# Kernel tuning notes

Hardware: AMD Instinct MI355X
Metric: run time of the kernel (lower is better)

The kernel has to match this reference:

```python
import jax, jax.numpy as jnp
import numpy as np

B, N, K = 32, 4096, 8          # batch, num input features (64x64 map), num slots
HID, D, DM = 256, 256, 512     # hid_dim, slot_dim, mlp_hid_dim
ITERS = 3
TEMP = 1.0
EPS = 1e-8
SCALE = D ** -0.5              # (slot_dim // num_heads) ** -0.5, heads=1


def layer_norm(x, g, b):
    m = jnp.mean(x, axis=-1, keepdims=True)
    v = jnp.mean((x - m) ** 2, axis=-1, keepdims=True)
    return (x - m) * jax.lax.rsqrt(v + 1e-5) * g + b


def setup_inputs() -> dict:
    key = jax.random.key(0)
    ks = jax.random.split(key, 20)
    s = 0.02
    inp = {
        "inputs": jax.random.normal(ks[0], (B, N, HID), jnp.float32),
        "noise": jax.random.normal(ks[1], (B, K, D), jnp.float32),
        "slots_mu": jax.random.normal(ks[2], (1, 1, D), jnp.float32),
        "slots_sigma": jnp.abs(jax.random.normal(ks[3], (1, 1, D), jnp.float32)),
        "ln_in_g": jnp.ones((HID,), jnp.float32),
        "ln_in_b": jnp.zeros((HID,), jnp.float32),
        "ln_slots_g": jnp.ones((D,), jnp.float32),
        "ln_slots_b": jnp.zeros((D,), jnp.float32),
        "ln_mlp_g": jnp.ones((D,), jnp.float32),
        "ln_mlp_b": jnp.zeros((D,), jnp.float32),
        # Linear weights stored [in, out]
        "Wq": jax.random.normal(ks[4], (D, D), jnp.float32) * s,
        "bq": jnp.zeros((D,), jnp.float32),
        "Wk": jax.random.normal(ks[5], (HID, D), jnp.float32) * s,
        "bk": jnp.zeros((D,), jnp.float32),
        "Wv": jax.random.normal(ks[6], (HID, D), jnp.float32) * s,
        "bv": jnp.zeros((D,), jnp.float32),
        # GRUCell params (torch layout transposed to [in, 3D])
        "W_ih": jax.random.normal(ks[7], (D, 3 * D), jnp.float32) * s,
        "W_hh": jax.random.normal(ks[8], (D, 3 * D), jnp.float32) * s,
        "b_ih": jnp.zeros((3 * D,), jnp.float32),
        "b_hh": jnp.zeros((3 * D,), jnp.float32),
        # residual MLP
        "W1": jax.random.normal(ks[9], (D, DM), jnp.float32) * s,
        "b1": jnp.zeros((DM,), jnp.float32),
        "W2": jax.random.normal(ks[10], (DM, D), jnp.float32) * s,
        "b2": jnp.zeros((D,), jnp.float32),
    }
    return inp


def reference(inputs, noise, slots_mu, slots_sigma,
              ln_in_g, ln_in_b, ln_slots_g, ln_slots_b, ln_mlp_g, ln_mlp_b,
              Wq, bq, Wk, bk, Wv, bv,
              W_ih, W_hh, b_ih, b_hh,
              W1, b1, W2, b2):
    x = layer_norm(inputs, ln_in_g, ln_in_b)            # [B,N,HID]
    k = x @ Wk + bk                                     # [B,N,D]
    v = x @ Wv + bv                                     # [B,N,D]

    slots = slots_mu + slots_sigma * noise              # [B,K,D]

    for _ in range(ITERS):
        slots_prev = slots
        s = layer_norm(slots, ln_slots_g, ln_slots_b)
        q = s @ Wq + bq                                  # [B,K,D]
        dots = jnp.einsum('bkd,bnd->bkn', q, k) * SCALE / TEMP
        attn = jax.nn.softmax(dots, axis=1)              # inverted: over slot axis
        attn = attn + EPS
        attn = attn / jnp.sum(attn, axis=2, keepdims=True)  # weighted mean over keys
        updates = jnp.einsum('bkn,bnd->bkd', attn, v)    # [B,K,D]

        # GRUCell on flattened (B*K, D)
        xg = updates.reshape(-1, D)
        h = slots_prev.reshape(-1, D)
        gi = xg @ W_ih + b_ih
        gh = h @ W_hh + b_hh
        i_r, i_z, i_n = jnp.split(gi, 3, axis=-1)
        h_r, h_z, h_n = jnp.split(gh, 3, axis=-1)
        r = jax.nn.sigmoid(i_r + h_r)
        z = jax.nn.sigmoid(i_z + h_z)
        n = jnp.tanh(i_n + r * h_n)
        h = (1.0 - z) * n + z * h
        slots = h.reshape(B, K, D)

        # residual MLP
        m = layer_norm(slots, ln_mlp_g, ln_mlp_b)
        slots = slots + (jax.nn.relu(m @ W1 + b1) @ W2 + b2)

    return slots
```

## Files before the change

### kernel.cpp

```cpp
#include <hip/hip_runtime.h>
#include <hip/hip_bf16.h>

#define NB 32
#define NPOS 4096
#define NSLOT 8
#define HIDD 256
#define DDIM 256
#define SCALE_F 0.0625f
#define EPS_F 1e-8f
#define NCHUNK 32
#define CPOS 128
#define TPOS 32

typedef __attribute__((ext_vector_type(4))) float f32x4;
typedef __attribute__((ext_vector_type(8))) short s16x8;
typedef __attribute__((ext_vector_type(2))) unsigned int u32x2;

__device__ __forceinline__ unsigned short f2bf(float f) {
    unsigned int x = __float_as_uint(f);
    x = (x + 0x7fffu + ((x >> 16) & 1u)) >> 16;
    return (unsigned short)x;
}
__device__ __forceinline__ float bf_lo(unsigned u) { return __uint_as_float(u << 16); }
__device__ __forceinline__ float bf_hi(unsigned u) { return __uint_as_float(u & 0xffff0000u); }

__global__ __launch_bounds__(256) void k_ln_in(
        const float* __restrict__ x, const float* __restrict__ g,
        const float* __restrict__ b, unsigned short* __restrict__ lnx) {
    int lane = threadIdx.x & 63;
    int wave = threadIdx.x >> 6;
    long row = (long)blockIdx.x * 4 + wave;
    const float4* xr = (const float4*)(x + row * 256);
    float4 v = xr[lane];
    float s = v.x + v.y + v.z + v.w;
    float sq = v.x * v.x + v.y * v.y + v.z * v.z + v.w * v.w;
    #pragma unroll
    for (int m = 32; m; m >>= 1) { s += __shfl_xor(s, m); sq += __shfl_xor(sq, m); }
    float mean = s * 0.00390625f;
    float rstd = rsqrtf(sq * 0.00390625f - mean * mean + 1e-5f);
    const float4 gg = ((const float4*)g)[lane];
    const float4 bb = ((const float4*)b)[lane];
    ushort4 o;
    o.x = f2bf((v.x - mean) * rstd * gg.x + bb.x);
    o.y = f2bf((v.y - mean) * rstd * gg.y + bb.y);
    o.z = f2bf((v.z - mean) * rstd * gg.z + bb.z);
    o.w = f2bf((v.w - mean) * rstd * gg.w + bb.w);
    ((ushort4*)(lnx + row * 256))[lane] = o;
}

__device__ __forceinline__ unsigned packrow(const float* __restrict__ W, int hp, int N, int c) {
    return (unsigned)f2bf(W[(2*hp)*N + c]) | ((unsigned)f2bf(W[(2*hp+1)*N + c]) << 16);
}

__global__ __launch_bounds__(256) void k_prep(
        const float* __restrict__ Wq, const float* __restrict__ Wk,
        const float* __restrict__ Wv, const float* __restrict__ Wih,
        const float* __restrict__ Whh, const float* __restrict__ W1,
        const float* __restrict__ W2,
        unsigned* __restrict__ WqP, unsigned* __restrict__ WkTP,
        unsigned* __restrict__ WvP, unsigned* __restrict__ WihP,
        unsigned* __restrict__ WhhP, unsigned* __restrict__ W1P,
        unsigned* __restrict__ W2P) {
    int i = blockIdx.x * 256 + threadIdx.x;
    if (i < 32768) {
        int hp = i >> 8, c = i & 255;
        WqP[i] = packrow(Wq, hp, 256, c);
        WvP[i] = packrow(Wv, hp, 256, c);
        WkTP[i] = (unsigned)f2bf(Wk[c*256 + 2*hp]) | ((unsigned)f2bf(Wk[c*256 + 2*hp + 1]) << 16);
    }
    if (i < 65536) {
        int hp1 = i >> 9, c1 = i & 511;
        W1P[i] = packrow(W1, hp1, 512, c1);
        int hp2 = i >> 8, c2 = i & 255;
        W2P[i] = packrow(W2, hp2, 256, c2);
    }
    if (i < 98304) {
        int hp = i / 768, c = i % 768;
        WihP[i] = packrow(Wih, hp, 768, c);
        WhhP[i] = packrow(Whh, hp, 768, c);
    }
}

__device__ __forceinline__ void qk_tail(
        float v0, float v1, int b, int s0,
        const float* __restrict__ lng, const float* __restrict__ lnb,
        const float* __restrict__ Wq, const float* __restrict__ bq,
        const float* __restrict__ Wk, const float* __restrict__ bk,
        unsigned short* __restrict__ qkg, float* __restrict__ qbkg,
        float (*sh)[256], float (*red)[4]) {
    int c = threadIdx.x;
    float s_0 = v0, q_0 = v0 * v0, s_1 = v1, q_1 = v1 * v1;
    #pragma unroll
    for (int m = 32; m; m >>= 1) {
        s_0 += __shfl_xor(s_0, m); q_0 += __shfl_xor(q_0, m);
        s_1 += __shfl_xor(s_1, m); q_1 += __shfl_xor(q_1, m);
    }
    if ((c & 63) == 0) { int w = c >> 6; red[w][0]=s_0; red[w][1]=q_0; red[w][2]=s_1; red[w][3]=q_1; }
    __syncthreads();
    float S0 = red[0][0]+red[1][0]+red[2][0]+red[3][0];
    float Q0 = red[0][1]+red[1][1]+red[2][1]+red[3][1];
    float S1 = red[0][2]+red[1][2]+red[2][2]+red[3][2];
    float Q1 = red[0][3]+red[1][3]+red[2][3]+red[3][3];
    float m0 = S0 * 0.00390625f, r0 = rsqrtf(Q0 * 0.00390625f - m0*m0 + 1e-5f);
    float m1 = S1 * 0.00390625f, r1 = rsqrtf(Q1 * 0.00390625f - m1*m1 + 1e-5f);
    float gc = lng[c], bc = lnb[c];
    sh[0][c] = (v0 - m0) * r0 * gc + bc;
    sh[1][c] = (v1 - m1) * r1 * gc + bc;
    __syncthreads();
    float qa0 = bq[c], qa1 = qa0;
    for (int h = 0; h < 256; h += 4) {
        float w0 = Wq[(h+0)*256+c], w1 = Wq[(h+1)*256+c];
        float w2 = Wq[(h+2)*256+c], w3 = Wq[(h+3)*256+c];
        float4 x0 = *(const float4*)&sh[0][h], x1 = *(const float4*)&sh[1][h];
        qa0 += x0.x*w0 + x0.y*w1 + x0.z*w2 + x0.w*w3;
        qa1 += x1.x*w0 + x1.y*w1 + x1.z*w2 + x1.w*w3;
    }
    __syncthreads();
    sh[0][c] = qa0; sh[1][c] = qa1;
    float bkc = bk[c];
    float p0 = qa0 * bkc, p1 = qa1 * bkc;
    #pragma unroll
    for (int m = 32; m; m >>= 1) { p0 += __shfl_xor(p0, m); p1 += __shfl_xor(p1, m); }
    __syncthreads();
    if ((c & 63) == 0) { int w = c >> 6; red[w][0] = p0; red[w][1] = p1; }
    __syncthreads();
    if (c < 2) qbkg[b*8 + s0 + c] = SCALE_F * (red[0][c]+red[1][c]+red[2][c]+red[3][c]);
    float k0 = 0.f, k1 = 0.f;
    const float* wkr = Wk + (long)c * 256;
    for (int d = 0; d < 256; d += 4) {
        float4 wk4 = *(const float4*)&wkr[d];
        float4 x0 = *(const float4*)&sh[0][d], x1 = *(const float4*)&sh[1][d];
        k0 += x0.x*wk4.x + x0.y*wk4.y + x0.z*wk4.z + x0.w*wk4.w;
        k1 += x1.x*wk4.x + x1.y*wk4.y + x1.z*wk4.z + x1.w*wk4.w;
    }
    qkg[(b*8 + s0    )*256 + c] = f2bf(SCALE_F * k0);
    qkg[(b*8 + s0 + 1)*256 + c] = f2bf(SCALE_F * k1);
}

__global__ __launch_bounds__(256) void k_init(
        const float* __restrict__ noise, const float* __restrict__ mu,
        const float* __restrict__ sig, const float* __restrict__ lng,
        const float* __restrict__ lnb, const float* __restrict__ Wq,
        const float* __restrict__ bq, const float* __restrict__ Wk,
        const float* __restrict__ bk, float* __restrict__ slots,
        unsigned short* __restrict__ qkg, float* __restrict__ qbkg) {
    __shared__ float sh[2][256];
    __shared__ float red[4][4];
    int b = blockIdx.x >> 2, rp = blockIdx.x & 3;
    int s0 = rp * 2, r0 = b * 8 + s0;
    int c = threadIdx.x;
    float v0 = mu[c] + sig[c] * noise[r0*256 + c];
    float v1 = mu[c] + sig[c] * noise[(r0+1)*256 + c];
    slots[r0*256 + c] = v0;
    slots[(r0+1)*256 + c] = v1;
    qk_tail(v0, v1, b, s0, lng, lnb, Wq, bq, Wk, bk, qkg, qbkg, sh, red);
}

__global__ __launch_bounds__(128) void k_stream(
        const unsigned short* __restrict__ lnx, const unsigned short* __restrict__ qk,
        const float* __restrict__ qbk, float* __restrict__ Upart,
        float* __restrict__ dpart) {
    __shared__ unsigned short xt[TPOS * 256];
    __shared__ float Ured[8 * 256];
    __shared__ float dred[8];
    int b = blockIdx.x >> 5, ch = blockIdx.x & 31;
    int t = threadIdx.x;
    int l = t & 63, w = t >> 6;
    for (int i = t; i < 2048; i += 128) Ured[i] = 0.f;
    if (t < 8) dred[t] = 0.f;
    int slot = l & 15, g = l >> 4;
    s16x8 qkf[8];
    float qbkv = 0.f;
    if (slot < 8) {
        const unsigned short* qrow = qk + (b*8 + slot) * 256;
        #pragma unroll
        for (int hk = 0; hk < 8; hk++)
            qkf[hk] = *(const s16x8*)(qrow + hk*32 + 8*g);
        qbkv = qbk[b*8 + slot];
    } else {
        #pragma unroll
        for (int hk = 0; hk < 8; hk++) qkf[hk] = (s16x8)0;
    }
    f32x4 uacc[16];
    #pragma unroll
    for (int i = 0; i < 16; i++) uacc[i] = (f32x4)0.f;
    float dreg = 0.f;
    int gbase = (b * NPOS + ch * CPOS) * 256;
    int pw = w * 16;
    __syncthreads();
    for (int tile = 0; tile < 4; tile++) {
        #pragma unroll
        for (int i = 0; i < 8; i++) {
            int c = t + 128 * i;
            int p = c >> 5, hc = c & 31;
            int4 v = *(const int4*)(lnx + gbase + (tile*TPOS + p)*256 + hc*8);
            *(int4*)&xt[p*256 + ((hc ^ (p & 15)) << 3)] = v;
        }
        __syncthreads();
        f32x4 acc = (f32x4)0.f;
        {
            int prow = pw + (l & 15);
            const unsigned short* xrow = &xt[prow * 256];
            int sw = prow & 15;
            #pragma unroll
            for (int hk = 0; hk < 8; hk++) {
                s16x8 a = *(const s16x8*)(xrow + (((hk*4 + g) ^ sw) << 3));
                acc = __builtin_amdgcn_mfma_f32_16x16x32_bf16(a, qkf[hk], acc, 0, 0, 0);
            }
        }
        float at[4];
        #pragma unroll
        for (int r = 0; r < 4; r++) {
            float v = acc[r] + qbkv;
            float m = v;
            m = fmaxf(m, __shfl_xor(m, 1));
            m = fmaxf(m, __shfl_xor(m, 2));
            m = fmaxf(m, __shfl_xor(m, 4));
            float e = __expf(v - m);
            float sum = e;
            sum += __shfl_xor(sum, 1);
            sum += __shfl_xor(sum, 2);
            sum += __shfl_xor(sum, 4);
            float a = e / sum;
            at[r] = a;
            dreg += a;
        }
        u32x2 a2;
        a2.x = (unsigned)f2bf(at[0]) | ((unsigned)f2bf(at[1]) << 16);
        a2.y = (unsigned)f2bf(at[2]) | ((unsigned)f2bf(at[3]) << 16);
        int p0 = pw + 4 * g;
        int hl = l & 7;
        #pragma unroll
        for (int hc = 0; hc < 16; hc++) {
            int hcol = hc * 2 + ((l & 15) >> 3);
            unsigned e0 = xt[(p0+0)*256 + ((hcol ^ ((p0+0) & 15)) << 3) + hl];
            unsigned e1 = xt[(p0+1)*256 + ((hcol ^ ((p0+1) & 15)) << 3) + hl];
            unsigned e2 = xt[(p0+2)*256 + ((hcol ^ ((p0+2) & 15)) << 3) + hl];
            unsigned e3 = xt[(p0+3)*256 + ((hcol ^ ((p0+3) & 15)) << 3) + hl];
            u32x2 b2;
            b2.x = e0 | (e1 << 16);
            b2.y = e2 | (e3 << 16);
            asm volatile("v_mfma_f32_16x16x16_bf16 %0, %1, %2, %0"
                         : "+v"(uacc[hc]) : "v"(a2), "v"(b2));
        }
        __syncthreads();
    }
    if (g < 2) {
        #pragma unroll
        for (int hc = 0; hc < 16; hc++) {
            int h = hc * 16 + (l & 15);
            #pragma unroll
            for (int r = 0; r < 4; r++)
                atomicAdd(&Ured[(4*g + r)*256 + h], uacc[hc][r]);
        }
    }
    dreg += __shfl_xor(dreg, 16);
    dreg += __shfl_xor(dreg, 32);
    if (slot < 8 && g == 0) atomicAdd(&dred[slot], dreg);
    __syncthreads();
    float* up = Upart + (long)(b * NCHUNK + ch) * 2048;
    for (int i = t; i < 2048; i += 128) up[i] = Ured[i];
    if (t < 8) dpart[(b * NCHUNK + ch) * 8 + t] = dred[t];
}

__device__ __forceinline__ float ln1024(float v, int c, const float* __restrict__ g,
                                        const float* __restrict__ b, float (*red)[2]) {
    float s1 = v, s2 = v * v;
    #pragma unroll
    for (int m = 32; m; m >>= 1) { s1 += __shfl_xor(s1, m); s2 += __shfl_xor(s2, m); }
    int w = threadIdx.x >> 6;
    if ((threadIdx.x & 63) == 0) { red[w][0] = s1; red[w][1] = s2; }
    __syncthreads();
    float S = 0.f, Q = 0.f;
    #pragma unroll
    for (int i = 0; i < 16; i++) { S += red[i][0]; Q += red[i][1]; }
    float mean = S * (1.f/1024.f);
    float rstd = rsqrtf(Q * (1.f/1024.f) - mean*mean + 1e-5f);
    __syncthreads();
    return (v - mean) * rstd * g[c] + b[c];
}

__global__ __launch_bounds__(1024) void k_post(
        const float* __restrict__ Upart, const float* __restrict__ dpart,
        const unsigned* __restrict__ WvP, const float* __restrict__ bv,
        const unsigned* __restrict__ WihP, const unsigned* __restrict__ WhhP,
        const float* __restrict__ bih, const float* __restrict__ bhh,
        const float* __restrict__ lnmg, const float* __restrict__ lnmb,
        const unsigned* __restrict__ W1P, const float* __restrict__ b1,
        const unsigned* __restrict__ W2P, const float* __restrict__ b2,
        const float* __restrict__ lnsg, const float* __restrict__ lnsb,
        const unsigned* __restrict__ WqP, const float* __restrict__ bq,
        const unsigned* __restrict__ WkTP, const float* __restrict__ bk,
        float* __restrict__ slots, unsigned short* __restrict__ qkg,
        float* __restrict__ qbkg, float* __restrict__ outp, int last) {
    __shared__ float A[256];
    __shared__ float B[256];
    __shared__ float P4[4][256];
    __shared__ float G[12][256];
    __shared__ float H2[2][512];
    __shared__ float H[512];
    __shared__ float red[16][2];
    __shared__ float scal[1];
    int r = blockIdx.x, b = r >> 3, s = r & 7;
    int t = threadIdx.x, c = t & 255, q = t >> 8;
    {
        float u = 0.f;
        const float* ub = Upart + (long)b * NCHUNK * 2048 + s * 256 + c;
        #pragma unroll
        for (int i = 0; i < 8; i++) u += ub[(q * 8 + i) * 2048];
        P4[q][c] = u;
        if (q == 1) B[c] = slots[r * 256 + c];
        if (t < 32) {
            float dv = dpart[(b * NCHUNK + t) * 8 + s];
            #pragma unroll
            for (int m = 16; m; m >>= 1) dv += __shfl_xor(dv, m);
            if (t == 0) scal[0] = dv;
        }
    }
    __syncthreads();
    float dn = 1.f / (scal[0] + (float)NPOS * EPS_F);
    if (q == 0) A[c] = P4[0][c] + P4[1][c] + P4[2][c] + P4[3][c];
    __syncthreads();
    {
        float acc = 0.f;
        const unsigned* wp = WvP + q * 32 * 256 + c;
        const float* ap = A + q * 64;
        #pragma unroll 8
        for (int i = 0; i < 32; i++) {
            unsigned wv = wp[i * 256];
            acc += ap[2*i] * bf_lo(wv) + ap[2*i+1] * bf_hi(wv);
        }
        P4[q][c] = acc;
    }
    __syncthreads();
    float updc = (P4[0][c] + P4[1][c] + P4[2][c] + P4[3][c]) * dn + bv[c];
    if (q == 0) A[c] = updc;
    __syncthreads();
    {
        const float* src = (q < 2) ? A : B;
        const unsigned* W = (q < 2) ? WihP : WhhP;
        int base = (q & 1) * 64;
        float ar = 0.f, az = 0.f, an = 0.f;
        #pragma unroll 4
        for (int i = 0; i < 64; i++) {
            int hp = base + i;
            float a0 = src[2*hp], a1 = src[2*hp+1];
            unsigned w0 = W[hp*768 + c];
            unsigned w1 = W[hp*768 + c + 256];
            unsigned w2 = W[hp*768 + c + 512];
            ar += a0*bf_lo(w0) + a1*bf_hi(w0);
            az += a0*bf_lo(w1) + a1*bf_hi(w1);
            an += a0*bf_lo(w2) + a1*bf_hi(w2);
        }
        G[q*3+0][c] = ar; G[q*3+1][c] = az; G[q*3+2][c] = an;
    }
    __syncthreads();
    float spc = B[c];
    float gir = bih[c]     + G[0][c] + G[3][c];
    float giz = bih[c+256] + G[1][c] + G[4][c];
    float gin = bih[c+512] + G[2][c] + G[5][c];
    float ghr = bhh[c]     + G[6][c] + G[9][c];
    float ghz = bhh[c+256] + G[7][c] + G[10][c];
    float ghn = bhh[c+512] + G[8][c] + G[11][c];
    float rg = 1.f/(1.f + __expf(-(gir+ghr)));
    float zg = 1.f/(1.f + __expf(-(giz+ghz)));
    float ng = tanhf(gin + rg*ghn);
    float hnew = (1.f - zg)*ng + zg*spc;
    float mmc = ln1024(hnew, c, lnmg, lnmb, red);
    if (q == 0) A[c] = mmc;
    __syncthreads();
    {
        int j = t & 511, kh = t >> 9;
        float acc = 0.f;
        #pragma unroll 8
        for (int i = 0; i < 64; i++) {
            int hp = kh*64 + i;
            unsigned wv = W1P[hp*512 + j];
            acc += A[2*hp]*bf_lo(wv) + A[2*hp+1]*bf_hi(wv);
        }
        H2[kh][j] = acc;
    }
    __syncthreads();
    if (t < 512) H[t] = fmaxf(H2[0][t] + H2[1][t] + b1[t], 0.f);
    __syncthreads();
    {
        float acc = 0.f;
        const unsigned* wp = W2P + q * 64 * 256 + c;
        const float* hb = H + q * 128;
        #pragma unroll 8
        for (int i = 0; i < 64; i++) {
            unsigned wv = wp[i * 256];
            acc += hb[2*i]*bf_lo(wv) + hb[2*i+1]*bf_hi(wv);
        }
        P4[q][c] = acc;
    }
    __syncthreads();
    float outc = hnew + P4[0][c] + P4[1][c] + P4[2][c] + P4[3][c] + b2[c];
    if (t < 256) {
        slots[r*256 + c] = outc;
        if (last) outp[r*256 + c] = outc;
    }
    if (last) return;
    float sc = ln1024(outc, c, lnsg, lnsb, red);
    if (q == 0) A[c] = sc;
    __syncthreads();
    {
        float acc = 0.f;
        const unsigned* wp = WqP + q * 32 * 256 + c;
        const float* ap = A + q * 64;
        #pragma unroll 8
        for (int i = 0; i < 32; i++) {
            unsigned wv = wp[i * 256];
            acc += ap[2*i]*bf_lo(wv) + ap[2*i+1]*bf_hi(wv);
        }
        P4[q][c] = acc;
    }
    __syncthreads();
    float qc = P4[0][c] + P4[1][c] + P4[2][c] + P4[3][c] + bq[c];
    {
        float v = qc * bk[c];
        #pragma unroll
        for (int m = 32; m; m >>= 1) v += __shfl_xor(v, m);
        int w = t >> 6;
        if ((t & 63) == 0) red[w][0] = v;
        __syncthreads();
        if (t == 0) {
            float S = 0.f;
            #pragma unroll
            for (int i = 0; i < 16; i++) S += red[i][0];
            qbkg[r] = SCALE_F * 0.25f * S;
        }
    }
    if (q == 0) A[c] = qc;
    __syncthreads();
    {
        float acc = 0.f;
        const unsigned* wp = WkTP + q * 32 * 256 + c;
        const float* ap = A + q * 64;
        #pragma unroll 8
        for (int i = 0; i < 32; i++) {
            unsigned wv = wp[i * 256];
            acc += ap[2*i]*bf_lo(wv) + ap[2*i+1]*bf_hi(wv);
        }
        P4[q][c] = acc;
    }
    __syncthreads();
    if (t < 256) qkg[r*256 + c] = f2bf(SCALE_F * (P4[0][c] + P4[1][c] + P4[2][c] + P4[3][c]));
}

extern "C" void kernel_launch(void* const* d_in, const int* in_sizes, int n_in,
                              void* d_out, int out_size, void* d_ws, size_t ws_size,
                              hipStream_t stream) {
    const float* inputs = (const float*)d_in[0];
    const float* noise  = (const float*)d_in[1];
    const float* mu     = (const float*)d_in[2];
    const float* sig    = (const float*)d_in[3];
    const float* lnig   = (const float*)d_in[4];
    const float* lnib   = (const float*)d_in[5];
    const float* lnsg   = (const float*)d_in[6];
    const float* lnsb   = (const float*)d_in[7];
    const float* lnmg   = (const float*)d_in[8];
    const float* lnmb   = (const float*)d_in[9];
    const float* Wq     = (const float*)d_in[10];
    const float* bq     = (const float*)d_in[11];
    const float* Wk     = (const float*)d_in[12];
    const float* bk     = (const float*)d_in[13];
    const float* Wv     = (const float*)d_in[14];
    const float* bv     = (const float*)d_in[15];
    const float* Wih    = (const float*)d_in[16];
    const float* Whh    = (const float*)d_in[17];
    const float* bih    = (const float*)d_in[18];
    const float* bhh    = (const float*)d_in[19];
    const float* W1     = (const float*)d_in[20];
    const float* b1     = (const float*)d_in[21];
    const float* W2     = (const float*)d_in[22];
    const float* b2     = (const float*)d_in[23];

    char* ws = (char*)d_ws;
    unsigned short* lnx = (unsigned short*)ws;
    size_t off = (size_t)NB * NPOS * HIDD * 2;
    unsigned short* qkb = (unsigned short*)(ws + off); off += (size_t)NB*NSLOT*HIDD*2;
    float* qbk   = (float*)(ws + off); off += (size_t)NB*NSLOT*4;
    float* Upart = (float*)(ws + off); off += (size_t)NB*NCHUNK*NSLOT*HIDD*4;
    float* dpart = (float*)(ws + off); off += (size_t)NB*NCHUNK*NSLOT*4;
    float* slots = (float*)(ws + off); off += (size_t)NB*NSLOT*DDIM*4;
    unsigned* WqP  = (unsigned*)(ws + off); off += 32768u*4;
    unsigned* WkTP = (unsigned*)(ws + off); off += 32768u*4;
    unsigned* WvP  = (unsigned*)(ws + off); off += 32768u*4;
    unsigned* WihP = (unsigned*)(ws + off); off += 98304u*4;
    unsigned* WhhP = (unsigned*)(ws + off); off += 98304u*4;
    unsigned* W1P  = (unsigned*)(ws + off); off += 65536u*4;
    unsigned* W2P  = (unsigned*)(ws + off); off += 65536u*4;

    k_prep<<<384, 256, 0, stream>>>(Wq, Wk, Wv, Wih, Whh, W1, W2,
                                    WqP, WkTP, WvP, WihP, WhhP, W1P, W2P);
    k_ln_in<<<NB*NPOS/4, 256, 0, stream>>>(inputs, lnig, lnib, lnx);
    k_init<<<NB*4, 256, 0, stream>>>(noise, mu, sig, lnsg, lnsb, Wq, bq, Wk, bk,
                                     slots, qkb, qbk);
    for (int it = 0; it < 3; it++) {
        k_stream<<<NB*NCHUNK, 128, 0, stream>>>(lnx, qkb, qbk, Upart, dpart);
        k_post<<<NB*NSLOT, 1024, 0, stream>>>(Upart, dpart,
                                              WvP, bv, WihP, WhhP, bih, bhh,
                                              lnmg, lnmb, W1P, b1, W2P, b2,
                                              lnsg, lnsb, WqP, bq, WkTP, bk,
                                              slots, qkb, qbk, (float*)d_out,
                                              it == 2 ? 1 : 0);
    }
}
```

Before: 242.9 us.

## Vectorize k_post matvecs with 16-byte weight loads and finer K-split reductions

Each matrix-vector product in the per-slot post kernel now has every thread load four packed bf16 weight columns with one uint4 access. The input dimension is split into 8 or 16 groups instead of 2 or 4, and the partial sums are reduced through a larger shared-memory union. The aim is fewer, wider global loads and more memory-level parallelism in the weight-bandwidth-bound GRU, MLP and q/k projections. In exchange it adds extra shared-memory reduction passes and barriers, and uses more LDS per block.

```diff
diff --git a/kernel.cpp b/kernel.cpp
--- a/kernel.cpp
+++ b/kernel.cpp
@@ -23,6 +23,13 @@
 }
 __device__ __forceinline__ float bf_lo(unsigned u) { return __uint_as_float(u << 16); }
 __device__ __forceinline__ float bf_hi(unsigned u) { return __uint_as_float(u & 0xffff0000u); }
+
+__device__ __forceinline__ void fma4(f32x4& acc, uint4 wv, float a0, float a1) {
+    acc[0] += a0 * bf_lo(wv.x) + a1 * bf_hi(wv.x);
+    acc[1] += a0 * bf_lo(wv.y) + a1 * bf_hi(wv.y);
+    acc[2] += a0 * bf_lo(wv.z) + a1 * bf_hi(wv.z);
+    acc[3] += a0 * bf_lo(wv.w) + a1 * bf_hi(wv.w);
+}
 
 __global__ __launch_bounds__(256) void k_ln_in(
         const float* __restrict__ x, const float* __restrict__ g,
@@ -293,22 +300,22 @@
         const unsigned* __restrict__ WkTP, const float* __restrict__ bk,
         float* __restrict__ slots, unsigned short* __restrict__ qkg,
         float* __restrict__ qbkg, float* __restrict__ outp, int last) {
-    __shared__ float A[256];
-    __shared__ float B[256];
-    __shared__ float P4[4][256];
-    __shared__ float G[12][256];
-    __shared__ float H2[2][512];
-    __shared__ float H[512];
+    __shared__ union {
+        float PG[2][8][768];
+        struct { float P16[16][256]; float H2[8][512]; } s;
+    } sm;
+    __shared__ float A[256], B[256], G2[2][768], H[512];
     __shared__ float red[16][2];
     __shared__ float scal[1];
     int r = blockIdx.x, b = r >> 3, s = r & 7;
     int t = threadIdx.x, c = t & 255, q = t >> 8;
+    int cg = t & 63, kg16 = t >> 6;
     {
         float u = 0.f;
         const float* ub = Upart + (long)b * NCHUNK * 2048 + s * 256 + c;
         #pragma unroll
         for (int i = 0; i < 8; i++) u += ub[(q * 8 + i) * 2048];
-        P4[q][c] = u;
+        sm.s.P16[q][c] = u;
         if (q == 1) B[c] = slots[r * 256 + c];
         if (t < 32) {
             float dv = dpart[(b * NCHUNK + t) * 8 + s];
@@ -319,49 +326,66 @@
     }
     __syncthreads();
     float dn = 1.f / (scal[0] + (float)NPOS * EPS_F);
-    if (q == 0) A[c] = P4[0][c] + P4[1][c] + P4[2][c] + P4[3][c];
-    __syncthreads();
-    {
-        float acc = 0.f;
-        const unsigned* wp = WvP + q * 32 * 256 + c;
-        const float* ap = A + q * 64;
-        #pragma unroll 8
-        for (int i = 0; i < 32; i++) {
-            unsigned wv = wp[i * 256];
-            acc += ap[2*i] * bf_lo(wv) + ap[2*i+1] * bf_hi(wv);
-        }
-        P4[q][c] = acc;
-    }
-    __syncthreads();
-    float updc = (P4[0][c] + P4[1][c] + P4[2][c] + P4[3][c]) * dn + bv[c];
-    if (q == 0) A[c] = updc;
-    __syncthreads();
-    {
-        const float* src = (q < 2) ? A : B;
-        const unsigned* W = (q < 2) ? WihP : WhhP;
-        int base = (q & 1) * 64;
-        float ar = 0.f, az = 0.f, an = 0.f;
+    if (q == 0) A[c] = sm.s.P16[0][c] + sm.s.P16[1][c] + sm.s.P16[2][c] + sm.s.P16[3][c];
+    __syncthreads();
+    {
+        f32x4 acc = (f32x4)0.f;
+        const uint4* wp = (const uint4*)(WvP + kg16 * 8 * 256 + 4 * cg);
+        #pragma unroll
+        for (int i = 0; i < 8; i++) {
+            uint4 wv = wp[i * 64];
+            fma4(acc, wv, A[2*(kg16*8+i)], A[2*(kg16*8+i)+1]);
+        }
+        *(f32x4*)&sm.s.P16[kg16][4*cg] = acc;
+    }
+    __syncthreads();
+    float updtmp;
+    {
+        float ss = 0.f;
+        #pragma unroll
+        for (int k = 0; k < 16; k++) ss += sm.s.P16[k][c];
+        updtmp = ss * dn + bv[c];
+    }
+    __syncthreads();
+    if (q == 0) A[c] = updtmp;
+    __syncthreads();
+    {
+        int h = t >> 9;
+        int kg = (t >> 6) & 7;
+        const float* src = h ? B : A;
+        const unsigned* W = h ? WhhP : WihP;
+        f32x4 ar = (f32x4)0.f, az = (f32x4)0.f, an = (f32x4)0.f;
         #pragma unroll 4
-        for (int i = 0; i < 64; i++) {
-            int hp = base + i;
+        for (int i = 0; i < 16; i++) {
+            int hp = kg * 16 + i;
             float a0 = src[2*hp], a1 = src[2*hp+1];
-            unsigned w0 = W[hp*768 + c];
-            unsigned w1 = W[hp*768 + c + 256];
-            unsigned w2 = W[hp*768 + c + 512];
-            ar += a0*bf_lo(w0) + a1*bf_hi(w0);
-            az += a0*bf_lo(w1) + a1*bf_hi(w1);
-            an += a0*bf_lo(w2) + a1*bf_hi(w2);
-        }
-        G[q*3+0][c] = ar; G[q*3+1][c] = az; G[q*3+2][c] = an;
+            uint4 w0 = *(const uint4*)(W + hp*768 + 4*cg);
+            uint4 w1 = *(const uint4*)(W + hp*768 + 256 + 4*cg);
+            uint4 w2 = *(const uint4*)(W + hp*768 + 512 + 4*cg);
+            fma4(ar, w0, a0, a1);
+            fma4(az, w1, a0, a1);
+            fma4(an, w2, a0, a1);
+        }
+        *(f32x4*)&sm.PG[h][kg][4*cg]       = ar;
+        *(f32x4*)&sm.PG[h][kg][256 + 4*cg] = az;
+        *(f32x4*)&sm.PG[h][kg][512 + 4*cg] = an;
+    }
+    __syncthreads();
+    for (int idx = t; idx < 1536; idx += 1024) {
+        int h = idx / 768, cc = idx - h * 768;
+        float ss = 0.f;
+        #pragma unroll
+        for (int k = 0; k < 8; k++) ss += sm.PG[h][k][cc];
+        G2[h][cc] = ss;
     }
     __syncthreads();
     float spc = B[c];
-    float gir = bih[c]     + G[0][c] + G[3][c];
-    float giz = bih[c+256] + G[1][c] + G[4][c];
-    float gin = bih[c+512] + G[2][c] + G[5][c];
-    float ghr = bhh[c]     + G[6][c] + G[9][c];
-    float ghz = bhh[c+256] + G[7][c] + G[10][c];
-    float ghn = bhh[c+512] + G[8][c] + G[11][c];
+    float gir = bih[c]     + G2[0][c];
+    float giz = bih[c+256] + G2[0][c+256];
+    float gin = bih[c+512] + G2[0][c+512];
+    float ghr = bhh[c]     + G2[1][c];
+    float ghz = bhh[c+256] + G2[1][c+256];
+    float ghn = bhh[c+512] + G2[1][c+512];
     float rg = 1.f/(1.f + __expf(-(gir+ghr)));
     float zg = 1.f/(1.f + __expf(-(giz+ghz)));
     float ng = tanhf(gin + rg*ghn);
@@ -370,53 +394,69 @@
     if (q == 0) A[c] = mmc;
     __syncthreads();
     {
-        int j = t & 511, kh = t >> 9;
-        float acc = 0.f;
-        #pragma unroll 8
-        for (int i = 0; i < 64; i++) {
-            int hp = kh*64 + i;
-            unsigned wv = W1P[hp*512 + j];
-            acc += A[2*hp]*bf_lo(wv) + A[2*hp+1]*bf_hi(wv);
-        }
-        H2[kh][j] = acc;
-    }
-    __syncthreads();
-    if (t < 512) H[t] = fmaxf(H2[0][t] + H2[1][t] + b1[t], 0.f);
-    __syncthreads();
-    {
-        float acc = 0.f;
-        const unsigned* wp = W2P + q * 64 * 256 + c;
-        const float* hb = H + q * 128;
-        #pragma unroll 8
-        for (int i = 0; i < 64; i++) {
-            unsigned wv = wp[i * 256];
-            acc += hb[2*i]*bf_lo(wv) + hb[2*i+1]*bf_hi(wv);
-        }
-        P4[q][c] = acc;
-    }
-    __syncthreads();
-    float outc = hnew + P4[0][c] + P4[1][c] + P4[2][c] + P4[3][c] + b2[c];
+        int kg = t >> 7, cg1 = t & 127;
+        f32x4 acc = (f32x4)0.f;
+        const uint4* wp = (const uint4*)(W1P + kg * 16 * 512 + 4 * cg1);
+        #pragma unroll 4
+        for (int i = 0; i < 16; i++) {
+            uint4 wv = wp[i * 128];
+            fma4(acc, wv, A[2*(kg*16+i)], A[2*(kg*16+i)+1]);
+        }
+        *(f32x4*)&sm.s.H2[kg][4*cg1] = acc;
+    }
+    __syncthreads();
+    if (t < 512) {
+        float ss = b1[t];
+        #pragma unroll
+        for (int k = 0; k < 8; k++) ss += sm.s.H2[k][t];
+        H[t] = fmaxf(ss, 0.f);
+    }
+    __syncthreads();
+    {
+        f32x4 acc = (f32x4)0.f;
+        const uint4* wp = (const uint4*)(W2P + kg16 * 16 * 256 + 4 * cg);
+        #pragma unroll 4
+        for (int i = 0; i < 16; i++) {
+            uint4 wv = wp[i * 64];
+            fma4(acc, wv, H[2*(kg16*16+i)], H[2*(kg16*16+i)+1]);
+        }
+        *(f32x4*)&sm.s.P16[kg16][4*cg] = acc;
+    }
+    __syncthreads();
+    float outc;
+    {
+        float ss = 0.f;
+        #pragma unroll
+        for (int k = 0; k < 16; k++) ss += sm.s.P16[k][c];
+        outc = hnew + ss + b2[c];
+    }
     if (t < 256) {
         slots[r*256 + c] = outc;
         if (last) outp[r*256 + c] = outc;
     }
     if (last) return;
+    __syncthreads();
     float sc = ln1024(outc, c, lnsg, lnsb, red);
     if (q == 0) A[c] = sc;
     __syncthreads();
     {
-        float acc = 0.f;
-        const unsigned* wp = WqP + q * 32 * 256 + c;
-        const float* ap = A + q * 64;
-        #pragma unroll 8
-        for (int i = 0; i < 32; i++) {
-            unsigned wv = wp[i * 256];
-            acc += ap[2*i]*bf_lo(wv) + ap[2*i+1]*bf_hi(wv);
-        }
-        P4[q][c] = acc;
-    }
-    __syncthreads();
-    float qc = P4[0][c] + P4[1][c] + P4[2][c] + P4[3][c] + bq[c];
+        f32x4 acc = (f32x4)0.f;
+        const uint4* wp = (const uint4*)(WqP + kg16 * 8 * 256 + 4 * cg);
+        #pragma unroll
+        for (int i = 0; i < 8; i++) {
+            uint4 wv = wp[i * 64];
+            fma4(acc, wv, A[2*(kg16*8+i)], A[2*(kg16*8+i)+1]);
+        }
+        *(f32x4*)&sm.s.P16[kg16][4*cg] = acc;
+    }
+    __syncthreads();
+    float qc;
+    {
+        float ss = 0.f;
+        #pragma unroll
+        for (int k = 0; k < 16; k++) ss += sm.s.P16[k][c];
+        qc = ss + bq[c];
+    }
     {
         float v = qc * bk[c];
         #pragma unroll
@@ -430,22 +470,27 @@
             for (int i = 0; i < 16; i++) S += red[i][0];
             qbkg[r] = SCALE_F * 0.25f * S;
         }
+        __syncthreads();
     }
     if (q == 0) A[c] = qc;
     __syncthreads();
     {
-        float acc = 0.f;
-        const unsigned* wp = WkTP + q * 32 * 256 + c;
-        const float* ap = A + q * 64;
-        #pragma unroll 8
-        for (int i = 0; i < 32; i++) {
-            unsigned wv = wp[i * 256];
-            acc += ap[2*i]*bf_lo(wv) + ap[2*i+1]*bf_hi(wv);
-        }
-        P4[q][c] = acc;
-    }
-    __syncthreads();
-    if (t < 256) qkg[r*256 + c] = f2bf(SCALE_F * (P4[0][c] + P4[1][c] + P4[2][c] + P4[3][c]));
+        f32x4 acc = (f32x4)0.f;
+        const uint4* wp = (const uint4*)(WkTP + kg16 * 8 * 256 + 4 * cg);
+        #pragma unroll
+        for (int i = 0; i < 8; i++) {
+            uint4 wv = wp[i * 64];
+            fma4(acc, wv, A[2*(kg16*8+i)], A[2*(kg16*8+i)+1]);
+        }
+        *(f32x4*)&sm.s.P16[kg16][4*cg] = acc;
+    }
+    __syncthreads();
+    if (t < 256) {
+        float ss = 0.f;
+        #pragma unroll
+        for (int k = 0; k < 16; k++) ss += sm.s.P16[k][c];
+        qkg[r*256 + c] = f2bf(SCALE_F * ss);
+    }
 }
 
 extern "C" void kernel_launch(void* const* d_in, const int* in_sizes, int n_in,
```

Result: faster. 236.6 us (-2.6%).

## Fold Wq·Wkᵀ into one matrix, batch 4 slots per post block, use fp16 dot2

Applied to the files above, without the earlier changes.

Precomputes the fused query-key projection M = Wq·Wkᵀ plus the bias terms once in the prep kernel, so the post kernel does one matvec for q·K where it used to do two. The post kernel now handles 4 slots per 1024-thread block (64 blocks instead of 256), so each weight load is reused across 4 slots. The matvecs use packed fp16 weights and fdot2 instead of bf16 unpacking. This reduces weight traffic and instruction count in the serial per-iteration post step. In exchange it uses far fewer blocks and fp16 for weights and activations, which risks overflow or precision loss.

```diff
diff --git a/kernel.cpp b/kernel.cpp
--- a/kernel.cpp
+++ b/kernel.cpp
@@ -15,14 +15,21 @@
 typedef __attribute__((ext_vector_type(4))) float f32x4;
 typedef __attribute__((ext_vector_type(8))) short s16x8;
 typedef __attribute__((ext_vector_type(2))) unsigned int u32x2;
+typedef _Float16 h16x2 __attribute__((ext_vector_type(2)));
 
 __device__ __forceinline__ unsigned short f2bf(float f) {
     unsigned int x = __float_as_uint(f);
     x = (x + 0x7fffu + ((x >> 16) & 1u)) >> 16;
     return (unsigned short)x;
 }
-__device__ __forceinline__ float bf_lo(unsigned u) { return __uint_as_float(u << 16); }
-__device__ __forceinline__ float bf_hi(unsigned u) { return __uint_as_float(u & 0xffff0000u); }
+__device__ __forceinline__ unsigned short f2h(float f) {
+    _Float16 h = (_Float16)f;
+    return __builtin_bit_cast(unsigned short, h);
+}
+__device__ __forceinline__ unsigned pack2h(float a, float b) {
+    return (unsigned)f2h(a) | ((unsigned)f2h(b) << 16);
+}
+__device__ __forceinline__ h16x2 u2h(unsigned u) { return __builtin_bit_cast(h16x2, u); }
 
 __global__ __launch_bounds__(256) void k_ln_in(
         const float* __restrict__ x, const float* __restrict__ g,
@@ -48,48 +55,89 @@
     ((ushort4*)(lnx + row * 256))[lane] = o;
 }
 
-__device__ __forceinline__ unsigned packrow(const float* __restrict__ W, int hp, int N, int c) {
-    return (unsigned)f2bf(W[(2*hp)*N + c]) | ((unsigned)f2bf(W[(2*hp+1)*N + c]) << 16);
+__device__ __forceinline__ unsigned packrowh(const float* __restrict__ W, int hp, int N, int c) {
+    return pack2h(W[(2*hp)*N + c], W[(2*hp+1)*N + c]);
+}
+__device__ __forceinline__ float blkred(float v, float* red4) {
+    #pragma unroll
+    for (int m = 32; m; m >>= 1) v += __shfl_xor(v, m);
+    int w = threadIdx.x >> 6;
+    if ((threadIdx.x & 63) == 0) red4[w] = v;
+    __syncthreads();
+    float s = red4[0] + red4[1] + red4[2] + red4[3];
+    __syncthreads();
+    return s;
 }
 
 __global__ __launch_bounds__(256) void k_prep(
-        const float* __restrict__ Wq, const float* __restrict__ Wk,
         const float* __restrict__ Wv, const float* __restrict__ Wih,
         const float* __restrict__ Whh, const float* __restrict__ W1,
-        const float* __restrict__ W2,
-        unsigned* __restrict__ WqP, unsigned* __restrict__ WkTP,
+        const float* __restrict__ W2, const float* __restrict__ Wq,
+        const float* __restrict__ Wk, const float* __restrict__ bq,
+        const float* __restrict__ bk,
         unsigned* __restrict__ WvP, unsigned* __restrict__ WihP,
         unsigned* __restrict__ WhhP, unsigned* __restrict__ W1P,
-        unsigned* __restrict__ W2P) {
-    int i = blockIdx.x * 256 + threadIdx.x;
-    if (i < 32768) {
-        int hp = i >> 8, c = i & 255;
-        WqP[i] = packrow(Wq, hp, 256, c);
-        WvP[i] = packrow(Wv, hp, 256, c);
-        WkTP[i] = (unsigned)f2bf(Wk[c*256 + 2*hp]) | ((unsigned)f2bf(Wk[c*256 + 2*hp + 1]) << 16);
-    }
-    if (i < 65536) {
-        int hp1 = i >> 9, c1 = i & 511;
-        W1P[i] = packrow(W1, hp1, 512, c1);
-        int hp2 = i >> 8, c2 = i & 255;
-        W2P[i] = packrow(W2, hp2, 256, c2);
-    }
-    if (i < 98304) {
-        int hp = i / 768, c = i % 768;
-        WihP[i] = packrow(Wih, hp, 768, c);
-        WhhP[i] = packrow(Whh, hp, 768, c);
+        unsigned* __restrict__ W2P, unsigned* __restrict__ M1P,
+        float* __restrict__ v1, float* __restrict__ w2, float* __restrict__ sc2) {
+    int t = threadIdx.x;
+    if (blockIdx.x < 384) {
+        int i = blockIdx.x * 256 + t;
+        if (i < 32768) {
+            int hp = i >> 8, c = i & 255;
+            WvP[i] = packrowh(Wv, hp, 256, c);
+        }
+        if (i < 65536) {
+            int hp1 = i >> 9, c1 = i & 511;
+            W1P[i] = packrowh(W1, hp1, 512, c1);
+            int hp2 = i >> 8, c2 = i & 255;
+            W2P[i] = packrowh(W2, hp2, 256, c2);
+        }
+        if (i < 98304) {
+            int hp = i / 768, c = i % 768;
+            WihP[i] = packrowh(Wih, hp, 768, c);
+            WhhP[i] = packrowh(Whh, hp, 768, c);
+        }
+        return;
+    }
+    __shared__ float wq0[256], wq1[256], bqL[256];
+    __shared__ float red4[4];
+    int e2 = blockIdx.x - 384;
+    wq0[t] = Wq[(2*e2)*256 + t];
+    wq1[t] = Wq[(2*e2+1)*256 + t];
+    bqL[t] = bq[t];
+    __syncthreads();
+    const float4* wkr = (const float4*)(Wk + (long)t * 256);
+    float a0 = 0.f, a1 = 0.f;
+    for (int d = 0; d < 64; d++) {
+        float4 k4 = wkr[d];
+        a0 += wq0[4*d]*k4.x + wq0[4*d+1]*k4.y + wq0[4*d+2]*k4.z + wq0[4*d+3]*k4.w;
+        a1 += wq1[4*d]*k4.x + wq1[4*d+1]*k4.y + wq1[4*d+2]*k4.z + wq1[4*d+3]*k4.w;
+    }
+    M1P[e2*256 + t] = pack2h(a0, a1);
+    float p0 = blkred(wq0[t] * bk[t], red4);
+    float p1 = blkred(wq1[t] * bk[t], red4);
+    if (t == 0) { w2[2*e2] = p0; w2[2*e2+1] = p1; }
+    if (e2 == 0) {
+        float av = 0.f;
+        for (int d = 0; d < 64; d++) {
+            float4 k4 = wkr[d];
+            av += bqL[4*d]*k4.x + bqL[4*d+1]*k4.y + bqL[4*d+2]*k4.z + bqL[4*d+3]*k4.w;
+        }
+        v1[t] = av;
+        float p2 = blkred(bqL[t] * bk[t], red4);
+        if (t == 0) sc2[0] = p2;
     }
 }
 
 __device__ __forceinline__ void qk_tail(
-        float v0, float v1, int b, int s0,
+        float v0, float v1_, int b, int s0,
         const float* __restrict__ lng, const float* __restrict__ lnb,
         const float* __restrict__ Wq, const float* __restrict__ bq,
         const float* __restrict__ Wk, const float* __restrict__ bk,
         unsigned short* __restrict__ qkg, float* __restrict__ qbkg,
         float (*sh)[256], float (*red)[4]) {
     int c = threadIdx.x;
-    float s_0 = v0, q_0 = v0 * v0, s_1 = v1, q_1 = v1 * v1;
+    float s_0 = v0, q_0 = v0 * v0, s_1 = v1_, q_1 = v1_ * v1_;
     #pragma unroll
     for (int m = 32; m; m >>= 1) {
         s_0 += __shfl_xor(s_0, m); q_0 += __shfl_xor(q_0, m);
@@ -105,15 +153,15 @@
     float m1 = S1 * 0.00390625f, r1 = rsqrtf(Q1 * 0.00390625f - m1*m1 + 1e-5f);
     float gc = lng[c], bc = lnb[c];
     sh[0][c] = (v0 - m0) * r0 * gc + bc;
-    sh[1][c] = (v1 - m1) * r1 * gc + bc;
+    sh[1][c] = (v1_ - m1) * r1 * gc + bc;
     __syncthreads();
     float qa0 = bq[c], qa1 = qa0;
     for (int h = 0; h < 256; h += 4) {
         float w0 = Wq[(h+0)*256+c], w1 = Wq[(h+1)*256+c];
-        float w2 = Wq[(h+2)*256+c], w3 = Wq[(h+3)*256+c];
+        float w2_ = Wq[(h+2)*256+c], w3 = Wq[(h+3)*256+c];
         float4 x0 = *(const float4*)&sh[0][h], x1 = *(const float4*)&sh[1][h];
-        qa0 += x0.x*w0 + x0.y*w1 + x0.z*w2 + x0.w*w3;
-        qa1 += x1.x*w0 + x1.y*w1 + x1.z*w2 + x1.w*w3;
+        qa0 += x0.x*w0 + x0.y*w1 + x0.z*w2_ + x0.w*w3;
+        qa1 += x1.x*w0 + x1.y*w1 + x1.z*w2_ + x1.w*w3;
     }
     __syncthreads();
     sh[0][c] = qa0; sh[1][c] = qa1;
@@ -263,19 +311,19 @@
     if (t < 8) dpart[(b * NCHUNK + ch) * 8 + t] = dred[t];
 }
 
-__device__ __forceinline__ float ln1024(float v, int c, const float* __restrict__ g,
-                                        const float* __restrict__ b, float (*red)[2]) {
+__device__ __forceinline__ float ln4r(float v, int s, int c, int w,
+                                      const float* __restrict__ g,
+                                      const float* __restrict__ b,
+                                      float (*red)[2]) {
     float s1 = v, s2 = v * v;
     #pragma unroll
     for (int m = 32; m; m >>= 1) { s1 += __shfl_xor(s1, m); s2 += __shfl_xor(s2, m); }
-    int w = threadIdx.x >> 6;
     if ((threadIdx.x & 63) == 0) { red[w][0] = s1; red[w][1] = s2; }
     __syncthreads();
-    float S = 0.f, Q = 0.f;
-    #pragma unroll
-    for (int i = 0; i < 16; i++) { S += red[i][0]; Q += red[i][1]; }
-    float mean = S * (1.f/1024.f);
-    float rstd = rsqrtf(Q * (1.f/1024.f) - mean*mean + 1e-5f);
+    float S = red[4*s][0] + red[4*s+1][0] + red[4*s+2][0] + red[4*s+3][0];
+    float Q = red[4*s][1] + red[4*s+1][1] + red[4*s+2][1] + red[4*s+3][1];
+    float mean = S * 0.00390625f;
+    float rstd = rsqrtf(Q * 0.00390625f - mean*mean + 1e-5f);
     __syncthreads();
     return (v - mean) * rstd * g[c] + b[c];
 }
@@ -289,163 +337,123 @@
         const unsigned* __restrict__ W1P, const float* __restrict__ b1,
         const unsigned* __restrict__ W2P, const float* __restrict__ b2,
         const float* __restrict__ lnsg, const float* __restrict__ lnsb,
-        const unsigned* __restrict__ WqP, const float* __restrict__ bq,
-        const unsigned* __restrict__ WkTP, const float* __restrict__ bk,
+        const unsigned* __restrict__ M1P, const float* __restrict__ v1,
+        const float* __restrict__ w2g, const float* __restrict__ sc2g,
         float* __restrict__ slots, unsigned short* __restrict__ qkg,
         float* __restrict__ qbkg, float* __restrict__ outp, int last) {
-    __shared__ float A[256];
-    __shared__ float B[256];
-    __shared__ float P4[4][256];
-    __shared__ float G[12][256];
-    __shared__ float H2[2][512];
-    __shared__ float H[512];
+    __shared__ float Us[4][256], sl[4][256], hn[4][256], mm[4][256];
+    __shared__ float Hh[4][512];
+    __shared__ unsigned ap[4][128], apS[4][128], apH[4][256];
     __shared__ float red[16][2];
-    __shared__ float scal[1];
-    int r = blockIdx.x, b = r >> 3, s = r & 7;
-    int t = threadIdx.x, c = t & 255, q = t >> 8;
+    __shared__ float dnl[4];
+    int b = blockIdx.x >> 1, sh = blockIdx.x & 1, s0 = sh * 4;
+    int t = threadIdx.x, c = t & 255, s = t >> 8, w = t >> 6;
     {
         float u = 0.f;
-        const float* ub = Upart + (long)b * NCHUNK * 2048 + s * 256 + c;
-        #pragma unroll
-        for (int i = 0; i < 8; i++) u += ub[(q * 8 + i) * 2048];
-        P4[q][c] = u;
-        if (q == 1) B[c] = slots[r * 256 + c];
-        if (t < 32) {
-            float dv = dpart[(b * NCHUNK + t) * 8 + s];
-            #pragma unroll
-            for (int m = 16; m; m >>= 1) dv += __shfl_xor(dv, m);
-            if (t == 0) scal[0] = dv;
-        }
-    }
-    __syncthreads();
-    float dn = 1.f / (scal[0] + (float)NPOS * EPS_F);
-    if (q == 0) A[c] = P4[0][c] + P4[1][c] + P4[2][c] + P4[3][c];
-    __syncthreads();
-    {
-        float acc = 0.f;
-        const unsigned* wp = WvP + q * 32 * 256 + c;
-        const float* ap = A + q * 64;
+        const float* ub = Upart + ((long)b * 256 + s0 + s) * 256 + c;
         #pragma unroll 8
-        for (int i = 0; i < 32; i++) {
-            unsigned wv = wp[i * 256];
-            acc += ap[2*i] * bf_lo(wv) + ap[2*i+1] * bf_hi(wv);
-        }
-        P4[q][c] = acc;
-    }
-    __syncthreads();
-    float updc = (P4[0][c] + P4[1][c] + P4[2][c] + P4[3][c]) * dn + bv[c];
-    if (q == 0) A[c] = updc;
-    __syncthreads();
-    {
-        const float* src = (q < 2) ? A : B;
-        const unsigned* W = (q < 2) ? WihP : WhhP;
-        int base = (q & 1) * 64;
-        float ar = 0.f, az = 0.f, an = 0.f;
-        #pragma unroll 4
-        for (int i = 0; i < 64; i++) {
-            int hp = base + i;
-            float a0 = src[2*hp], a1 = src[2*hp+1];
-            unsigned w0 = W[hp*768 + c];
-            unsigned w1 = W[hp*768 + c + 256];
-            unsigned w2 = W[hp*768 + c + 512];
-            ar += a0*bf_lo(w0) + a1*bf_hi(w0);
-            az += a0*bf_lo(w1) + a1*bf_hi(w1);
-            an += a0*bf_lo(w2) + a1*bf_hi(w2);
-        }
-        G[q*3+0][c] = ar; G[q*3+1][c] = az; G[q*3+2][c] = an;
-    }
-    __syncthreads();
-    float spc = B[c];
-    float gir = bih[c]     + G[0][c] + G[3][c];
-    float giz = bih[c+256] + G[1][c] + G[4][c];
-    float gin = bih[c+512] + G[2][c] + G[5][c];
-    float ghr = bhh[c]     + G[6][c] + G[9][c];
-    float ghz = bhh[c+256] + G[7][c] + G[10][c];
-    float ghn = bhh[c+512] + G[8][c] + G[11][c];
-    float rg = 1.f/(1.f + __expf(-(gir+ghr)));
-    float zg = 1.f/(1.f + __expf(-(giz+ghz)));
-    float ng = tanhf(gin + rg*ghn);
-    float hnew = (1.f - zg)*ng + zg*spc;
-    float mmc = ln1024(hnew, c, lnmg, lnmb, red);
-    if (q == 0) A[c] = mmc;
-    __syncthreads();
-    {
-        int j = t & 511, kh = t >> 9;
+        for (int ch = 0; ch < 32; ch++) u += ub[ch * 2048];
+        Us[s][c] = u;
+        sl[s][c] = slots[(b*8 + s0 + s)*256 + c];
+        if (t < 4) {
+            float d = 0.f;
+            for (int ch = 0; ch < 32; ch++) d += dpart[(b*32 + ch)*8 + s0 + t];
+            dnl[t] = 1.f / (d + (float)NPOS * EPS_F);
+        }
+    }
+    __syncthreads();
+    if (t < 512) { int ss = t >> 7, dp = t & 127; ap[ss][dp]  = pack2h(Us[ss][2*dp], Us[ss][2*dp+1]); }
+    else         { int ss = (t-512) >> 7, dp = t & 127; apS[ss][dp] = pack2h(sl[ss][2*dp], sl[ss][2*dp+1]); }
+    __syncthreads();
+    {
         float acc = 0.f;
         #pragma unroll 8
-        for (int i = 0; i < 64; i++) {
-            int hp = kh*64 + i;
-            unsigned wv = W1P[hp*512 + j];
-            acc += A[2*hp]*bf_lo(wv) + A[2*hp+1]*bf_hi(wv);
-        }
-        H2[kh][j] = acc;
-    }
-    __syncthreads();
-    if (t < 512) H[t] = fmaxf(H2[0][t] + H2[1][t] + b1[t], 0.f);
-    __syncthreads();
+        for (int dp = 0; dp < 128; dp++)
+            acc = __builtin_amdgcn_fdot2(u2h(ap[s][dp]), u2h(WvP[dp*256 + c]), acc, false);
+        mm[s][c] = acc * dnl[s] + bv[c];
+    }
+    __syncthreads();
+    if (t < 512) { int ss = t >> 7, dp = t & 127; ap[ss][dp] = pack2h(mm[ss][2*dp], mm[ss][2*dp+1]); }
+    __syncthreads();
+    float hnew;
+    {
+        float gir = bih[c], giz = bih[c+256], gin = bih[c+512];
+        float ghr = bhh[c], ghz = bhh[c+256], ghn = bhh[c+512];
+        const unsigned* wi = WihP + c;
+        const unsigned* wh = WhhP + c;
+        #pragma unroll 2
+        for (int dp = 0; dp < 128; dp++) {
+            h16x2 au = u2h(ap[s][dp]);
+            h16x2 as_ = u2h(apS[s][dp]);
+            gir = __builtin_amdgcn_fdot2(au, u2h(wi[dp*768]),       gir, false);
+            giz = __builtin_amdgcn_fdot2(au, u2h(wi[dp*768 + 256]), giz, false);
+            gin = __builtin_amdgcn_fdot2(au, u2h(wi[dp*768 + 512]), gin, false);
+            ghr = __builtin_amdgcn_fdot2(as_, u2h(wh[dp*768]),       ghr, false);
+            ghz = __builtin_amdgcn_fdot2(as_, u2h(wh[dp*768 + 256]), ghz, false);
+            ghn = __builtin_amdgcn_fdot2(as_, u2h(wh[dp*768 + 512]), ghn, false);
+        }
+        float rg = 1.f/(1.f + __expf(-(gir+ghr)));
+        float zg = 1.f/(1.f + __expf(-(giz+ghz)));
+        float ng = tanhf(gin + rg*ghn);
+        hnew = (1.f - zg)*ng + zg*sl[s][c];
+        hn[s][c] = hnew;
+    }
+    __syncthreads();
+    {
+        float mmv = ln4r(hnew, s, c, w, lnmg, lnmb, red);
+        mm[s][c] = mmv;
+    }
+    __syncthreads();
+    if (t < 512) { int ss = t >> 7, dp = t & 127; ap[ss][dp] = pack2h(mm[ss][2*dp], mm[ss][2*dp+1]); }
+    __syncthreads();
+    {
+        int j = t & 511, sp = t >> 9;
+        float a0 = b1[j], a1 = b1[j];
+        #pragma unroll 4
+        for (int dp = 0; dp < 128; dp++) {
+            h16x2 wv = u2h(W1P[dp*512 + j]);
+            a0 = __builtin_amdgcn_fdot2(u2h(ap[sp*2][dp]),   wv, a0, false);
+            a1 = __builtin_amdgcn_fdot2(u2h(ap[sp*2+1][dp]), wv, a1, false);
+        }
+        Hh[sp*2][j]   = fmaxf(a0, 0.f);
+        Hh[sp*2+1][j] = fmaxf(a1, 0.f);
+    }
+    __syncthreads();
+    { int hp = t & 255; apH[s][hp] = pack2h(Hh[s][2*hp], Hh[s][2*hp+1]); }
+    __syncthreads();
+    float outc;
     {
         float acc = 0.f;
-        const unsigned* wp = W2P + q * 64 * 256 + c;
-        const float* hb = H + q * 128;
         #pragma unroll 8
-        for (int i = 0; i < 64; i++) {
-            unsigned wv = wp[i * 256];
-            acc += hb[2*i]*bf_lo(wv) + hb[2*i+1]*bf_hi(wv);
-        }
-        P4[q][c] = acc;
-    }
-    __syncthreads();
-    float outc = hnew + P4[0][c] + P4[1][c] + P4[2][c] + P4[3][c] + b2[c];
-    if (t < 256) {
-        slots[r*256 + c] = outc;
-        if (last) outp[r*256 + c] = outc;
-    }
-    if (last) return;
-    float sc = ln1024(outc, c, lnsg, lnsb, red);
-    if (q == 0) A[c] = sc;
-    __syncthreads();
-    {
-        float acc = 0.f;
-        const unsigned* wp = WqP + q * 32 * 256 + c;
-        const float* ap = A + q * 64;
+        for (int hp = 0; hp < 256; hp++)
+            acc = __builtin_amdgcn_fdot2(u2h(apH[s][hp]), u2h(W2P[hp*256 + c]), acc, false);
+        outc = hn[s][c] + acc + b2[c];
+    }
+    slots[(b*8 + s0 + s)*256 + c] = outc;
+    if (last) { outp[(b*8 + s0 + s)*256 + c] = outc; return; }
+    __syncthreads();
+    {
+        float sc = ln4r(outc, s, c, w, lnsg, lnsb, red);
+        mm[s][c] = sc;
+        float qv = sc * w2g[c];
+        #pragma unroll
+        for (int m = 32; m; m >>= 1) qv += __shfl_xor(qv, m);
+        if ((t & 63) == 0) red[w][0] = qv;
+    }
+    __syncthreads();
+    if (t < 512) { int ss = t >> 7, dp = t & 127; ap[ss][dp] = pack2h(mm[ss][2*dp], mm[ss][2*dp+1]); }
+    if ((t & 255) == 0) {
+        float S = red[4*s][0] + red[4*s+1][0] + red[4*s+2][0] + red[4*s+3][0];
+        qbkg[b*8 + s0 + s] = SCALE_F * (S + sc2g[0]);
+    }
+    __syncthreads();
+    {
+        float acc = v1[c];
         #pragma unroll 8
-        for (int i = 0; i < 32; i++) {
-            unsigned wv = wp[i * 256];
-            acc += ap[2*i]*bf_lo(wv) + ap[2*i+1]*bf_hi(wv);
-        }
-        P4[q][c] = acc;
-    }
-    __syncthreads();
-    float qc = P4[0][c] + P4[1][c] + P4[2][c] + P4[3][c] + bq[c];
-    {
-        float v = qc * bk[c];
-        #pragma unroll
-        for (int m = 32; m; m >>= 1) v += __shfl_xor(v, m);
-        int w = t >> 6;
-        if ((t & 63) == 0) red[w][0] = v;
-        __syncthreads();
-        if (t == 0) {
-            float S = 0.f;
-            #pragma unroll
-            for (int i = 0; i < 16; i++) S += red[i][0];
-            qbkg[r] = SCALE_F * 0.25f * S;
-        }
-    }
-    if (q == 0) A[c] = qc;
-    __syncthreads();
-    {
-        float acc = 0.f;
-        const unsigned* wp = WkTP + q * 32 * 256 + c;
-        const float* ap = A + q * 64;
-        #pragma unroll 8
-        for (int i = 0; i < 32; i++) {
-            unsigned wv = wp[i * 256];
-            acc += ap[2*i]*bf_lo(wv) + ap[2*i+1]*bf_hi(wv);
-        }
-        P4[q][c] = acc;
-    }
-    __syncthreads();
-    if (t < 256) qkg[r*256 + c] = f2bf(SCALE_F * (P4[0][c] + P4[1][c] + P4[2][c] + P4[3][c]));
+        for (int dp = 0; dp < 128; dp++)
+            acc = __builtin_amdgcn_fdot2(u2h(ap[s][dp]), u2h(M1P[dp*256 + c]), acc, false);
+        qkg[(b*8 + s0 + s)*256 + c] = f2bf(SCALE_F * acc);
+    }
 }
 
 extern "C" void kernel_launch(void* const* d_in, const int* in_sizes, int n_in,
@@ -484,26 +492,28 @@
     float* Upart = (float*)(ws + off); off += (size_t)NB*NCHUNK*NSLOT*HIDD*4;
     float* dpart = (float*)(ws + off); off += (size_t)NB*NCHUNK*NSLOT*4;
     float* slots = (float*)(ws + off); off += (size_t)NB*NSLOT*DDIM*4;
-    unsigned* WqP  = (unsigned*)(ws + off); off += 32768u*4;
-    unsigned* WkTP = (unsigned*)(ws + off); off += 32768u*4;
     unsigned* WvP  = (unsigned*)(ws + off); off += 32768u*4;
     unsigned* WihP = (unsigned*)(ws + off); off += 98304u*4;
     unsigned* WhhP = (unsigned*)(ws + off); off += 98304u*4;
     unsigned* W1P  = (unsigned*)(ws + off); off += 65536u*4;
     unsigned* W2P  = (unsigned*)(ws + off); off += 65536u*4;
-
-    k_prep<<<384, 256, 0, stream>>>(Wq, Wk, Wv, Wih, Whh, W1, W2,
-                                    WqP, WkTP, WvP, WihP, WhhP, W1P, W2P);
+    unsigned* M1P  = (unsigned*)(ws + off); off += 32768u*4;
+    float* v1   = (float*)(ws + off); off += 256*4;
+    float* w2   = (float*)(ws + off); off += 256*4;
+    float* sc2  = (float*)(ws + off); off += 64;
+
+    k_prep<<<512, 256, 0, stream>>>(Wv, Wih, Whh, W1, W2, Wq, Wk, bq, bk,
+                                    WvP, WihP, WhhP, W1P, W2P, M1P, v1, w2, sc2);
     k_ln_in<<<NB*NPOS/4, 256, 0, stream>>>(inputs, lnig, lnib, lnx);
     k_init<<<NB*4, 256, 0, stream>>>(noise, mu, sig, lnsg, lnsb, Wq, bq, Wk, bk,
                                      slots, qkb, qbk);
     for (int it = 0; it < 3; it++) {
         k_stream<<<NB*NCHUNK, 128, 0, stream>>>(lnx, qkb, qbk, Upart, dpart);
-        k_post<<<NB*NSLOT, 1024, 0, stream>>>(Upart, dpart,
-                                              WvP, bv, WihP, WhhP, bih, bhh,
-                                              lnmg, lnmb, W1P, b1, W2P, b2,
-                                              lnsg, lnsb, WqP, bq, WkTP, bk,
-                                              slots, qkb, qbk, (float*)d_out,
-                                              it == 2 ? 1 : 0);
-    }
-}
+        k_post<<<NB*2, 1024, 0, stream>>>(Upart, dpart,
+                                          WvP, bv, WihP, WhhP, bih, bhh,
+                                          lnmg, lnmb, W1P, b1, W2P, b2,
+                                          lnsg, lnsb, M1P, v1, w2, sc2,
+                                          slots, qkb, qbk, (float*)d_out,
+                                          it == 2 ? 1 : 0);
+    }
+}
```

New measurement: 360.3 us. +48.4%, slower.
